# Kernel tuning notes

Measured on AMD Instinct MI355X. Metric: run time of the kernel, lower is better.

The kernel has to match this reference:

```python
import jax, jax.numpy as jnp
import numpy as np

N_POINTS, N_GRIDS, K = 1024, 512, 7


def setup_inputs() -> dict:
    key = jax.random.key(0)
    k1, k2, k3, k4 = jax.random.split(key, 4)
    points = jax.random.uniform(k1, (N_POINTS, 3), dtype=jnp.float32) * 2.0 - 1.0
    volume_centers = jax.random.uniform(k2, (N_GRIDS, 3), dtype=jnp.float32) * 2.0 - 1.0
    min_s, max_s = 0.01, 1.0
    scales = jax.random.uniform(k3, (N_GRIDS,), dtype=jnp.float32) * (max_s - min_s) + min_s
    mosaic_sdf_values = jax.random.normal(k4, (N_GRIDS, K, K, K), dtype=jnp.float32)
    return {"points": points, "volume_centers": volume_centers,
            "scales": scales, "mosaic_sdf_values": mosaic_sdf_values}


def reference(points, volume_centers, scales, mosaic_sdf_values):
    G, k = mosaic_sdf_values.shape[0], mosaic_sdf_values.shape[1]
    # scaled relative positions: (N, G, 3)
    rel = (points[:, None, :] - volume_centers[None, :, :]) / scales[None, :, None]
    # grid node coordinates in [0,1]^3, flattened: (k^3, 3)
    lin = jnp.linspace(0.0, 1.0, k, dtype=points.dtype)
    gx, gy, gz = jnp.meshgrid(lin, lin, lin, indexing='ij')
    coords = jnp.stack([gx, gy, gz], axis=-1).reshape(-1, 3)
    # squared distance ||rel - coord||^2 expanded -> avoids (N,G,k^3,3) materialization
    d2 = (jnp.sum(rel * rel, axis=-1)[..., None]
          - 2.0 * jnp.einsum('ngd,cd->ngc', rel, coords)
          + jnp.sum(coords * coords, axis=-1)[None, None, :])  # (N, G, k^3)
    dist = jnp.sqrt(jnp.maximum(d2, 0.0))
    # original: weight = dist where dist <= 1 else 0, normalized over grid nodes
    w = jnp.where(dist <= 1.0, dist, 0.0)
    s = jnp.sum(w, axis=-1, keepdims=True)
    w = jnp.where(s > 0, w / jnp.where(s == 0, 1.0, s), 0.0)  # nan_to_num(0) equivalent
    vals = mosaic_sdf_values.reshape(G, -1)  # (G, k^3)
    interp = jnp.einsum('ngc,gc->ng', w, vals)  # (N, G)
    # per-grid blend weight: relu(1 - ||rel||), normalized over grids
    pdist = jnp.linalg.norm(rel, axis=-1)  # (N, G)
    gw = jax.nn.relu(1.0 - pdist)
    gs = jnp.sum(gw, axis=-1, keepdims=True)
    gw = jnp.where(gs > 0, gw / jnp.where(gs == 0, 1.0, gs), 0.0)
    return jnp.sum(interp * gw, axis=-1)  # (N,)
```

## Files before the change

kernel.cpp:

```cpp
#include <hip/hip_runtime.h>


#define NPTS   1024
#define NGRIDS 512
#define TPB    256
#define NBLK   512
#define ROWF   344
#define STEP   (1.0f / 6.0f)
#define FSQRT(x) __builtin_amdgcn_sqrtf(x)

__global__ __launch_bounds__(TPB) void msdf_fused(
    const float* __restrict__ points,
    const float* __restrict__ centers,
    const float* __restrict__ scales,
    const float* __restrict__ vals,
    float* __restrict__ out)
{
    __shared__ float  s_v[32][ROWF];
    __shared__ float4 s_pair[4][256];
    __shared__ unsigned short s_gid[4][256];
    __shared__ int   s_c[4];
    __shared__ float s_d[4];
    __shared__ float s_red[4][2];

    const int bid  = blockIdx.x;
    const int t    = threadIdx.x;
    const int w    = t >> 6;
    const int lane = t & 63;
    const int grp  = t >> 3;
    const int sub  = t & 7;

    float* s_cen = &s_v[0][0];
    float* s_scl = s_cen + 1536;
    {
        float4* dst = (float4*)s_cen;
        const float4* c4 = (const float4*)centers;
        const float4* s4 = (const float4*)scales;
        dst[t] = (t < 384) ? c4[t] : s4[t - 384];
        const int u = t + 256;
        dst[u] = (u < 384) ? c4[u] : s4[u - 384];
    }

    const int   p  = w >> 1;
    const int   n  = (bid << 1) + p;
    const float px = points[n * 3 + 0];
    const float py = points[n * 3 + 1];
    const float pz = points[n * 3 + 2];
    __syncthreads();

    float dsum  = 0.0f;
    int   cbase = 0;
    #pragma unroll
    for (int r = 0; r < 4; ++r) {
        const int g = ((w & 1) << 8) + (r << 6) + lane;
        const float invs = 1.0f / s_scl[g];
        const float rx = (px - s_cen[g * 3 + 0]) * invs;
        const float ry = (py - s_cen[g * 3 + 1]) * invs;
        const float rz = (pz - s_cen[g * 3 + 2]) * invs;
        const float gwr = 1.0f - FSQRT(rx * rx + ry * ry + rz * rz);
        const bool  act = (gwr > 0.0f);
        const unsigned long long m = __ballot(act);
        if (act) {
            const int pos = cbase + (int)__popcll(m & ((1ull << lane) - 1ull));
            s_pair[w][pos] = make_float4(rx, ry, rz, gwr);
            s_gid[w][pos]  = (unsigned short)g;
            dsum += gwr;
        }
        cbase += (int)__popcll(m);
    }
    #pragma unroll
    for (int o = 32; o >= 1; o >>= 1) dsum += __shfl_xor(dsum, o);
    if (lane == 0) { s_c[w] = cbase; s_d[w] = dsum; }
    __syncthreads();

    const int o1 = s_c[0];
    const int o2 = o1 + s_c[1];
    const int o3 = o2 + s_c[2];
    const int CT = o3 + s_c[3];
    const float den0 = s_d[0] + s_d[1];
    const float den1 = s_d[2] + s_d[3];

    float acc0 = 0.0f, acc1 = 0.0f;
    if (CT > 0) {
        const int nch = (CT + 31) >> 5;
        float  rbuf[43];
        float4 pr;
        int    gid, seg;

        #define FETCH(a_) {                                               \
            const int pc = ((a_) < CT) ? (a_) : (CT - 1);                 \
            seg = (pc >= o1) + (pc >= o2) + (pc >= o3);                   \
            const int b0 = (seg == 0) ? 0 : (seg == 1) ? o1               \
                         : (seg == 2) ? o2 : o3;                          \
            pr  = s_pair[seg][pc - b0];                                   \
            gid = (int)s_gid[seg][pc - b0]; }

        #define LOADROW() {                                               \
            const float* __restrict__ grow = vals + gid * 343;            \
            _Pragma("unroll")                                             \
            for (int k = 0; k < 42; ++k) rbuf[k] = grow[sub + 8 * k];     \
            rbuf[42] = (sub < 7) ? grow[336 + sub] : 0.0f; }

        FETCH(grp); LOADROW();
        float* __restrict__ myv = &s_v[grp][0];

        for (int c = 0; c < nch; ++c) {
            #pragma unroll
            for (int k = 0; k < 42; ++k) myv[sub + 8 * k] = rbuf[k];
            if (sub < 7) myv[336 + sub] = rbuf[42];

            const float4 prc  = pr;
            const int    segc = seg;
            const float  gw   = (32 * c + grp < CT) ? prc.w : 0.0f;

            if (c + 1 < nch) { FETCH(32 * (c + 1) + grp); LOADROW(); }

            float dy2[7], dz2[7];
            #pragma unroll
            for (int j = 0; j < 7; ++j) { const float d = prc.y - j * STEP; dy2[j] = d * d; }
            #pragma unroll
            for (int l = 0; l < 7; ++l) { const float d = prc.z - l * STEP; dz2[l] = d * d; }

            const int   slab = (sub < 7) ? sub : 6;
            const float dxv  = prc.x - slab * STEP;
            const float dx2  = (sub < 7) ? dxv * dxv : 4.0f;
            const float* __restrict__ vrow = myv + slab * 49;

            float ws = 0.0f, vs = 0.0f;
            #pragma unroll
            for (int j = 0; j < 7; ++j) {
                const float dxy = dx2 + dy2[j];
                #pragma unroll
                for (int l = 0; l < 7; ++l) {
                    const float d2 = dxy + dz2[l];
                    const float wt = (d2 <= 1.0f) ? FSQRT(d2) : 0.0f;
                    ws += wt;
                    vs  = fmaf(wt, vrow[j * 7 + l], vs);
                }
            }
            #pragma unroll
            for (int o = 4; o >= 1; o >>= 1) {
                ws += __shfl_xor(ws, o);
                vs += __shfl_xor(vs, o);
            }
            const float interp = (ws > 0.0f) ? (vs / ws) : 0.0f;
            if (sub == 0) {
                const float contrib = interp * gw;
                if (segc < 2) acc0 += contrib;
                else          acc1 += contrib;
            }
        }
        #undef FETCH
        #undef LOADROW
    }

    #pragma unroll
    for (int o = 32; o >= 1; o >>= 1) {
        acc0 += __shfl_xor(acc0, o);
        acc1 += __shfl_xor(acc1, o);
    }
    if (lane == 0) { s_red[w][0] = acc0; s_red[w][1] = acc1; }
    __syncthreads();
    if (t < 2) {
        const float nm = s_red[0][t] + s_red[1][t] + s_red[2][t] + s_red[3][t];
        const float dn = (t == 0) ? den0 : den1;
        out[(bid << 1) + t] = (dn > 0.0f) ? (nm / dn) : 0.0f;
    }
}

extern "C" void kernel_launch(void* const* d_in, const int* in_sizes, int n_in,
                              void* d_out, int out_size, void* d_ws, size_t ws_size,
                              hipStream_t stream) {
    const float* points  = (const float*)d_in[0];
    const float* centers = (const float*)d_in[1];
    const float* scales  = (const float*)d_in[2];
    const float* vals    = (const float*)d_in[3];
    float* out = (float*)d_out;

    msdf_fused<<<NBLK, TPB, 0, stream>>>(points, centers, scales, vals, out);
}
```

Baseline: 16.06 us.

## Double block size to 512 threads and split each grid row over 16 lanes

Doubles threads per block, so each point uses four waves for grid culling instead of two. Each active grid's 343 values are now handled by 16 lanes instead of 8: lanes take flattened (i,j) rows, use a magic-multiply divide by 7 to recover i and j, and handle the last partial row separately. The aim is to shorten the per-grid serial work and to halve the register prefetch buffer, raising parallelism and latency hiding. In exchange, the segment lookup and reductions are longer, the block has more waves to synchronise, and the row split leaves lanes unevenly loaded.

```diff
diff --git a/kernel.cpp b/kernel.cpp
--- a/kernel.cpp
+++ b/kernel.cpp
@@ -3,7 +3,7 @@
 
 #define NPTS   1024
 #define NGRIDS 512
-#define TPB    256
+#define TPB    512
 #define NBLK   512
 #define ROWF   344
 #define STEP   (1.0f / 6.0f)
@@ -17,18 +17,18 @@
     float* __restrict__ out)
 {
     __shared__ float  s_v[32][ROWF];
-    __shared__ float4 s_pair[4][256];
-    __shared__ unsigned short s_gid[4][256];
-    __shared__ int   s_c[4];
-    __shared__ float s_d[4];
-    __shared__ float s_red[4][2];
+    __shared__ float4 s_pair[8][128];
+    __shared__ unsigned short s_gid[8][128];
+    __shared__ int   s_c[8];
+    __shared__ float s_d[8];
+    __shared__ float s_red[8][2];
 
     const int bid  = blockIdx.x;
     const int t    = threadIdx.x;
     const int w    = t >> 6;
     const int lane = t & 63;
-    const int grp  = t >> 3;
-    const int sub  = t & 7;
+    const int grp  = t >> 4;
+    const int sub  = t & 15;
 
     float* s_cen = &s_v[0][0];
     float* s_scl = s_cen + 1536;
@@ -37,12 +37,9 @@
         const float4* c4 = (const float4*)centers;
         const float4* s4 = (const float4*)scales;
         dst[t] = (t < 384) ? c4[t] : s4[t - 384];
-        const int u = t + 256;
-        dst[u] = (u < 384) ? c4[u] : s4[u - 384];
     }
 
-    const int   p  = w >> 1;
-    const int   n  = (bid << 1) + p;
+    const int   n  = (bid << 1) + (w >> 2);
     const float px = points[n * 3 + 0];
     const float py = points[n * 3 + 1];
     const float pz = points[n * 3 + 2];
@@ -51,8 +48,8 @@
     float dsum  = 0.0f;
     int   cbase = 0;
     #pragma unroll
-    for (int r = 0; r < 4; ++r) {
-        const int g = ((w & 1) << 8) + (r << 6) + lane;
+    for (int r = 0; r < 2; ++r) {
+        const int g = ((w & 3) << 7) + (r << 6) + lane;
         const float invs = 1.0f / s_scl[g];
         const float rx = (px - s_cen[g * 3 + 0]) * invs;
         const float ry = (py - s_cen[g * 3 + 1]) * invs;
@@ -76,38 +73,45 @@
     const int o1 = s_c[0];
     const int o2 = o1 + s_c[1];
     const int o3 = o2 + s_c[2];
-    const int CT = o3 + s_c[3];
-    const float den0 = s_d[0] + s_d[1];
-    const float den1 = s_d[2] + s_d[3];
+    const int o4 = o3 + s_c[3];
+    const int o5 = o4 + s_c[4];
+    const int o6 = o5 + s_c[5];
+    const int o7 = o6 + s_c[6];
+    const int CT = o7 + s_c[7];
+    const float den0 = s_d[0] + s_d[1] + s_d[2] + s_d[3];
+    const float den1 = s_d[4] + s_d[5] + s_d[6] + s_d[7];
 
     float acc0 = 0.0f, acc1 = 0.0f;
     if (CT > 0) {
         const int nch = (CT + 31) >> 5;
-        float  rbuf[43];
+        float  rbuf[22];
         float4 pr;
         int    gid, seg;
 
         #define FETCH(a_) {                                               \
             const int pc = ((a_) < CT) ? (a_) : (CT - 1);                 \
-            seg = (pc >= o1) + (pc >= o2) + (pc >= o3);                   \
+            seg = (pc >= o1) + (pc >= o2) + (pc >= o3) + (pc >= o4)       \
+                + (pc >= o5) + (pc >= o6) + (pc >= o7);                   \
             const int b0 = (seg == 0) ? 0 : (seg == 1) ? o1               \
-                         : (seg == 2) ? o2 : o3;                          \
+                         : (seg == 2) ? o2 : (seg == 3) ? o3              \
+                         : (seg == 4) ? o4 : (seg == 5) ? o5              \
+                         : (seg == 6) ? o6 : o7;                          \
             pr  = s_pair[seg][pc - b0];                                   \
             gid = (int)s_gid[seg][pc - b0]; }
 
         #define LOADROW() {                                               \
             const float* __restrict__ grow = vals + gid * 343;            \
             _Pragma("unroll")                                             \
-            for (int k = 0; k < 42; ++k) rbuf[k] = grow[sub + 8 * k];     \
-            rbuf[42] = (sub < 7) ? grow[336 + sub] : 0.0f; }
+            for (int k = 0; k < 21; ++k) rbuf[k] = grow[sub + 16 * k];    \
+            rbuf[21] = (sub < 7) ? grow[336 + sub] : 0.0f; }
 
         FETCH(grp); LOADROW();
         float* __restrict__ myv = &s_v[grp][0];
 
         for (int c = 0; c < nch; ++c) {
             #pragma unroll
-            for (int k = 0; k < 42; ++k) myv[sub + 8 * k] = rbuf[k];
-            if (sub < 7) myv[336 + sub] = rbuf[42];
+            for (int k = 0; k < 21; ++k) myv[sub + 16 * k] = rbuf[k];
+            if (sub < 7) myv[336 + sub] = rbuf[21];
 
             const float4 prc  = pr;
             const int    segc = seg;
@@ -115,38 +119,46 @@
 
             if (c + 1 < nch) { FETCH(32 * (c + 1) + grp); LOADROW(); }
 
-            float dy2[7], dz2[7];
-            #pragma unroll
-            for (int j = 0; j < 7; ++j) { const float d = prc.y - j * STEP; dy2[j] = d * d; }
+            float dz2[7];
             #pragma unroll
             for (int l = 0; l < 7; ++l) { const float d = prc.z - l * STEP; dz2[l] = d * d; }
 
-            const int   slab = (sub < 7) ? sub : 6;
-            const float dxv  = prc.x - slab * STEP;
-            const float dx2  = (sub < 7) ? dxv * dxv : 4.0f;
-            const float* __restrict__ vrow = myv + slab * 49;
-
             float ws = 0.0f, vs = 0.0f;
             #pragma unroll
-            for (int j = 0; j < 7; ++j) {
-                const float dxy = dx2 + dy2[j];
+            for (int rr = 0; rr < 3; ++rr) {
+                const int rowid = sub + (rr << 4);
+                const int i = (rowid * 9363) >> 16;
+                const int j = rowid - i * 7;
+                const float dxv = prc.x - (float)i * STEP;
+                const float dyv = prc.y - (float)j * STEP;
+                const float dxy = dxv * dxv + dyv * dyv;
+                const float* __restrict__ vr = myv + rowid * 7;
                 #pragma unroll
                 for (int l = 0; l < 7; ++l) {
                     const float d2 = dxy + dz2[l];
                     const float wt = (d2 <= 1.0f) ? FSQRT(d2) : 0.0f;
                     ws += wt;
-                    vs  = fmaf(wt, vrow[j * 7 + l], vs);
+                    vs  = fmaf(wt, vr[l], vs);
                 }
             }
+            if (sub < 7) {
+                const float dxv = prc.x - 1.0f;
+                const float dyv = prc.y - 1.0f;
+                const float dzv = prc.z - (float)sub * STEP;
+                const float d2  = dxv * dxv + dyv * dyv + dzv * dzv;
+                const float wt  = (d2 <= 1.0f) ? FSQRT(d2) : 0.0f;
+                ws += wt;
+                vs  = fmaf(wt, myv[336 + sub], vs);
+            }
             #pragma unroll
-            for (int o = 4; o >= 1; o >>= 1) {
+            for (int o = 8; o >= 1; o >>= 1) {
                 ws += __shfl_xor(ws, o);
                 vs += __shfl_xor(vs, o);
             }
             const float interp = (ws > 0.0f) ? (vs / ws) : 0.0f;
             if (sub == 0) {
                 const float contrib = interp * gw;
-                if (segc < 2) acc0 += contrib;
+                if (segc < 4) acc0 += contrib;
                 else          acc1 += contrib;
             }
         }
@@ -162,7 +174,9 @@
     if (lane == 0) { s_red[w][0] = acc0; s_red[w][1] = acc1; }
     __syncthreads();
     if (t < 2) {
-        const float nm = s_red[0][t] + s_red[1][t] + s_red[2][t] + s_red[3][t];
+        float nm = 0.0f;
+        #pragma unroll
+        for (int i = 0; i < 8; ++i) nm += s_red[i][t];
         const float dn = (t == 0) ? den0 : den1;
         out[(bid << 1) + t] = (dn > 0.0f) ? (nm / dn) : 0.0f;
     }
```

New measurement: 16.54 us. 3.0% more time.
